# Optimization experiments

Measured on AMD Instinct MI355X. Metric: run time of the kernel, lower is better.

Reference implementation:

```python
import jax, jax.numpy as jnp
import numpy as np

B, S, D = 2, 8192, 2048
H, HD = 16, 128
LSH_NUM_PROJS = 7
BLOCK = 256          # key/query block size for block-diagonal attention
SAMPLE = 256         # number of uniformly sampled residual columns
ROPE_BASE = 10000.0
LOG_WEIGHT = float(np.log(S / SAMPLE))  # importance weight for sampled columns


def setup_inputs() -> dict:
    key = jax.random.key(0)
    ks = jax.random.split(key, 5)
    x = jax.random.normal(ks[0], (B, S, D), jnp.float32)
    w_in = jax.random.normal(ks[1], (D, 3 * D), jnp.float32) * (D ** -0.5)
    w_out = jax.random.normal(ks[2], (D, D), jnp.float32) * (D ** -0.5)
    lsh_proj = jax.random.normal(ks[3], (HD, LSH_NUM_PROJS), jnp.float32)
    sampled_set = jax.random.randint(ks[4], (B, H, SAMPLE), 0, S, jnp.int32)
    return {"x": x, "w_in": w_in, "w_out": w_out,
            "lsh_proj": lsh_proj, "sampled_set": sampled_set}


def _rope(t):
    # t: [B, S, H, HD]; LLaMA-style half-split rotary embedding, offset=0
    half = HD // 2
    inv_freq = 1.0 / (ROPE_BASE ** (jnp.arange(half, dtype=jnp.float32) / half))
    freqs = jnp.arange(S, dtype=jnp.float32)[:, None] * inv_freq[None, :]  # [S, half]
    cos = jnp.cos(freqs)[None, :, None, :]
    sin = jnp.sin(freqs)[None, :, None, :]
    t1, t2 = t[..., :half], t[..., half:]
    return jnp.concatenate([t1 * cos - t2 * sin, t2 * cos + t1 * sin], axis=-1)


def _lse_attn(q, k, v, scale, bias=None):
    # exact attention with log-sum-exp; q [...,n,d], k/v [...,m,d]
    s = jnp.einsum('...nd,...md->...nm', q, k) * scale
    if bias is not None:
        s = s + bias
    lse = jax.nn.logsumexp(s, axis=-1, keepdims=True)   # [...,n,1]
    p = jnp.exp(s - lse)
    return jnp.einsum('...nm,...md->...nd', p, v), lse


def _hyper_attention(q, k, v, lsh_proj, sampled_set):
    # q,k,v: [B,H,S,HD]  (non-causal HyperAttention path)
    scale = HD ** -0.5

    def lsh_hash(t):
        # simhash bucket codes from sign bits of random projections
        bits = jnp.einsum('bhsd,dp->bhsp', t, lsh_proj) > 0
        powers = (2 ** jnp.arange(LSH_NUM_PROJS)).astype(jnp.int32)
        return jnp.sum(bits.astype(jnp.int32) * powers, axis=-1)  # [B,H,S]

    q_idx = jnp.argsort(lsh_hash(q), axis=-1, stable=True)
    k_idx = jnp.argsort(lsh_hash(k), axis=-1, stable=True)
    q_idx_inv = jnp.argsort(q_idx, axis=-1, stable=True)
    gather = lambda t, i: jnp.take_along_axis(t, i[..., None], axis=2)

    qs = gather(q, q_idx)
    ks_ = gather(k, k_idx)
    vs = gather(v, k_idx)

    # 1. block-diagonal exact attention on LSH-sorted order
    nb = S // BLOCK
    qb = qs.reshape(B, H, nb, BLOCK, HD)
    kb = ks_.reshape(B, H, nb, BLOCK, HD)
    vb = vs.reshape(B, H, nb, BLOCK, HD)
    attn_blk, lse_blk = _lse_attn(qb, kb, vb, scale)
    attn_blk = attn_blk.reshape(B, H, S, HD)
    lse_blk = lse_blk.reshape(B, H, S, 1)

    # 2. residual: uniformly sampled columns (indices into sorted key order),
    #    masking columns already covered by the query's diagonal block
    k_sub = gather(ks_, sampled_set)   # [B,H,m,HD]
    v_sub = gather(vs, sampled_set)
    q_block_id = jnp.arange(S, dtype=jnp.int32) // BLOCK          # [S]
    s_block_id = sampled_set // BLOCK                             # [B,H,m]
    neg = jnp.finfo(q.dtype).min
    bias = jnp.where(q_block_id[None, None, :, None] == s_block_id[:, :, None, :],
                     neg, jnp.array(0.0, q.dtype))                # [B,H,S,m]
    attn_res, lse_res = _lse_attn(qs, k_sub, v_sub, scale, bias=bias)
    lse_res = lse_res + LOG_WEIGHT

    # 3. merge the two partial softmax results (online-softmax combine)
    lse = jnp.logaddexp(lse_blk, lse_res)
    attn = attn_blk * jnp.exp(lse_blk - lse) + attn_res * jnp.exp(lse_res - lse)

    # undo query sort
    return gather(attn, q_idx_inv)


def reference(x, w_in, w_out, lsh_proj, sampled_set):
    qkv = x @ w_in                           # [B,S,3D]
    q, k, v = jnp.split(qkv, 3, axis=-1)
    r4 = lambda t: t.reshape(B, S, H, HD)
    q, k, v = _rope(r4(q)), _rope(r4(k)), r4(v)
    tr = lambda t: t.transpose(0, 2, 1, 3)   # -> [B,H,S,HD]
    out = _hyper_attention(tr(q), tr(k), tr(v), lsh_proj, sampled_set)
    out = out.transpose(0, 2, 1, 3).reshape(B, S, D)
    return out @ w_out
```

## Files before the change

kernel.cpp:

```cpp
#include <hip/hip_runtime.h>
#include <stdint.h>

typedef _Float16 f16;
typedef _Float16 f16x8 __attribute__((ext_vector_type(8)));
typedef float f32x4 __attribute__((ext_vector_type(4)));
typedef uint32_t u32;

#define SEQ 8192
#define NH 16
#define HDIM 128
#define BHCNT 32
#define KDIM 2048
#define SCALE 0.08838834764831845f
#define LOGW 3.4657359027997265f
#define TAU1 0.06f
#define TAU 6e-3f
#define MAXWL 32768
#define BCAP 1024

__device__ __forceinline__ f32x4 mfma16(f16x8 a, f16x8 b, f32x4 c){
  return __builtin_amdgcn_mfma_f32_16x16x32_f16(a, b, c, 0, 0, 0);
}

__device__ __forceinline__ void g2l16(const f16* g, f16* l){
  __builtin_amdgcn_global_load_lds(
      (const __attribute__((address_space(1))) void*)g,
      (__attribute__((address_space(3))) void*)l, 16, 0, 0);
}

__global__ __launch_bounds__(256) void split_x_k(const float* __restrict__ x,
                                                 f16* __restrict__ xh, f16* __restrict__ xl){
  size_t i = ((size_t)blockIdx.x * 256 + threadIdx.x) * 4;
  float4 v = *(const float4*)(x + i);
  f16 h0 = (f16)v.x, h1 = (f16)v.y, h2 = (f16)v.z, h3 = (f16)v.w;
  union { f16 h[4]; ushort4 u; } a, b;
  a.h[0]=h0; a.h[1]=h1; a.h[2]=h2; a.h[3]=h3;
  b.h[0]=(f16)(v.x-(float)h0); b.h[1]=(f16)(v.y-(float)h1);
  b.h[2]=(f16)(v.z-(float)h2); b.h[3]=(f16)(v.w-(float)h3);
  *(ushort4*)(xh + i) = a.u;
  *(ushort4*)(xl + i) = b.u;
}

__global__ void transpose_k(const float* __restrict__ in, f16* __restrict__ ohi,
                            f16* __restrict__ olo, int Kd, int Nd, int NLO){
  __shared__ float t[32][33];
  int tx = threadIdx.x, ty = threadIdx.y;
  int n0 = blockIdx.x*32, k0 = blockIdx.y*32;
  #pragma unroll
  for (int i=0;i<4;i++) t[ty+i*8][tx] = in[(size_t)(k0+ty+i*8)*Nd + n0+tx];
  __syncthreads();
  #pragma unroll
  for (int i=0;i<4;i++){
    int n = n0 + ty + i*8, k = k0 + tx;
    float v = t[tx][ty+i*8];
    f16 h = (f16)v;
    ohi[(size_t)n*Kd + k] = h;
    if (n < NLO) olo[(size_t)n*Kd + k] = (f16)(v - (float)h);
  }
}

__global__ __launch_bounds__(256) void rope_table_k(float* __restrict__ ct, float* __restrict__ st){
  int i = blockIdx.x * 256 + threadIdx.x;
  int s = i >> 6, d = i & 63;
  float p32 = (float)pow(10000.0, (double)d / 64.0);
  float inv = __fdiv_rn(1.0f, p32);
  float f = __fmul_rn((float)s, inv);
  double a = (double)f;
  ct[i] = (float)cos(a);
  st[i] = (float)sin(a);
}

__global__ void zero_k(int* p){ p[0] = 0; p[1] = 0; p[2] = 0; }

__global__ void diag_k(const int* __restrict__ flags, float* __restrict__ out){
  int c = flags[0];
  if (c == 0 || c >= MAXWL || flags[2]) out[0] = 1.0e9f + (float)c;
}

template<int SPLIT, int MODE>
__global__ __launch_bounds__(256) void gemm_k(
    const f16* __restrict__ A, const f16* __restrict__ Al,
    const f16* __restrict__ Bt, const f16* __restrict__ Btl,
    float* __restrict__ o0, float* __restrict__ o1, f16* __restrict__ oh, int N){
  __shared__ f16 sm[SPLIT ? 16384 : 8192];
  const int tid = threadIdx.x, lane = tid & 63, wave = tid >> 6;
  const int wr = wave >> 1, wc = wave & 1;
  const int brow = blockIdx.y, bcol = blockIdx.x;
  const int g = lane >> 4, q_ = lane & 15;
  f32x4 acc[4][4];
  #pragma unroll
  for (int m=0;m<4;m++)
    #pragma unroll
    for (int n=0;n<4;n++) acc[m][n] = (f32x4){0.f,0.f,0.f,0.f};
  const int srow = tid >> 2, sseg = tid & 3;
  const int scol = (sseg ^ (srow & 3)) * 8;
  const f16* ga0 = A  + (size_t)(brow*128 + srow)*KDIM + scol;
  const f16* gb0 = Bt + (size_t)(bcol*128 + srow)*KDIM + scol;
  f16* As = sm; f16* Bs = sm + 4096;
  f16* dA0 = As + wave*512; f16* dA1 = As + 2048 + wave*512;
  f16* dB0 = Bs + wave*512; f16* dB1 = Bs + 2048 + wave*512;
  const int aoff = (wr*64 + q_)*32 + (g ^ (q_ & 3))*8;
  const int boff = (wc*64 + q_)*32 + (g ^ (q_ & 3))*8;
  for (int kt = 0; kt < KDIM/32; ++kt){
    const size_t ko = (size_t)kt * 32;
    g2l16(ga0 + ko, dA0); g2l16(ga0 + (size_t)64*KDIM + ko, dA1);
    g2l16(gb0 + ko, dB0); g2l16(gb0 + (size_t)64*KDIM + ko, dB1);
    if constexpr (SPLIT){
      const f16* gal = Al  + (ga0 - A);
      const f16* gbl = Btl + (gb0 - Bt);
      g2l16(gal + ko, sm + 8192  + wave*512); g2l16(gal + (size_t)64*KDIM + ko, sm + 8192  + 2048 + wave*512);
      g2l16(gbl + ko, sm + 12288 + wave*512); g2l16(gbl + (size_t)64*KDIM + ko, sm + 12288 + 2048 + wave*512);
    }
    __syncthreads();
    f16x8 af[4], afl[4];
    #pragma unroll
    for (int m=0;m<4;m++){
      af[m] = *(const f16x8*)&As[aoff + m*16*32];
      if constexpr (SPLIT) afl[m] = *(const f16x8*)&sm[8192 + aoff + m*16*32];
    }
    #pragma unroll
    for (int n=0;n<4;n++){
      f16x8 bf = *(const f16x8*)&Bs[boff + n*16*32];
      f16x8 bfl;
      if constexpr (SPLIT) bfl = *(const f16x8*)&sm[12288 + boff + n*16*32];
      #pragma unroll
      for (int m=0;m<4;m++){
        acc[m][n] = mfma16(af[m], bf, acc[m][n]);
        if constexpr (SPLIT){
          acc[m][n] = mfma16(af[m],  bfl, acc[m][n]);
          acc[m][n] = mfma16(afl[m], bf,  acc[m][n]);
        }
      }
    }
    __syncthreads();
  }
  #pragma unroll
  for (int m=0;m<4;m++)
    #pragma unroll
    for (int n=0;n<4;n++)
      #pragma unroll
      for (int j=0;j<4;j++){
        int row = brow*128 + wr*64 + m*16 + g*4 + j;
        int col = bcol*128 + wc*64 + n*16 + q_;
        float v = acc[m][n][j];
        if constexpr (MODE == 0){
          o0[(size_t)row * N + col] = v;
        } else if constexpr (MODE == 1){
          int b = row >> 13, s = row & 8191;
          int cl = col & 2047;
          int h = cl >> 7, hd = cl & 127;
          float* dst = (col < 2048) ? o0 : o1;
          dst[(((size_t)b*NH + h)*SEQ + s)*HDIM + hd] = v;
        } else {
          int b = row >> 13, s = row & 8191;
          int h = col >> 7, hd = col & 127;
          oh[(((size_t)b*NH + h)*SEQ + s)*HDIM + hd] = (f16)v;
        }
      }
}

__global__ __launch_bounds__(256) void rope_hash_k(float* __restrict__ qk, const float* __restrict__ ct,
    const float* __restrict__ st, const float* __restrict__ proj, int* __restrict__ hout,
    int tag, int* __restrict__ wl, int* __restrict__ wcnt){
  const int lane = threadIdx.x & 63, wave = threadIdx.x >> 6;
  const int s = blockIdx.x * 4 + wave, bh = blockIdx.y;
  float* row = qk + ((size_t)bh * SEQ + s) * HDIM;
  float2 v = *(const float2*)(row + 2*lane);
  float ox = __shfl_xor(v.x, 32), oy = __shfl_xor(v.y, 32);
  const int dl = 2*lane, di = dl & 63;
  const float* cb = ct + (size_t)s*64; const float* sb = st + (size_t)s*64;
  float c0 = cb[di], c1 = cb[di+1], sn0 = sb[di], sn1 = sb[di+1];
  float r0, r1;
  if (lane < 32){ r0 = v.x*c0 - ox*sn0; r1 = v.y*c1 - oy*sn1; }
  else          { r0 = v.x*c0 + ox*sn0; r1 = v.y*c1 + oy*sn1; }
  union { f16 h[2]; u32 u; } pk;
  pk.h[0] = (f16)r0; pk.h[1] = (f16)r1;
  *(u32*)((f16*)row + dl) = pk.u;
  float part[7];
  #pragma unroll
  for (int p=0;p<7;p++) part[p] = r0*proj[dl*7+p] + r1*proj[(dl+1)*7+p];
  #pragma unroll
  for (int off=32; off>=1; off>>=1){
    #pragma unroll
    for (int p=0;p<7;p++) part[p] += __shfl_xor(part[p], off);
  }
  if (lane == 0){
    int hs = 0; float mn = 1e30f;
    #pragma unroll
    for (int p=0;p<7;p++){ if (part[p] > 0.f) hs |= (1<<p); mn = fminf(mn, fabsf(part[p])); }
    hout[bh*SEQ + s] = hs;
    if (mn < TAU1){
      int w = atomicAdd(wcnt, 1);
      if (w < MAXWL){ wl[2*w] = (bh<<1) | tag; wl[2*w+1] = s; }
    }
  }
}

__global__ __launch_bounds__(256) void bucket_k(const int* __restrict__ wl, const int* __restrict__ wcnt,
    int* __restrict__ wl2, int* __restrict__ cnt2, int* __restrict__ flags){
  const int bucket = blockIdx.x;
  __shared__ int lcnt;
  if (threadIdx.x == 0) lcnt = 0;
  __syncthreads();
  int count = wcnt[0]; if (count > MAXWL) count = MAXWL;
  for (int i = threadIdx.x; i < count; i += 256){
    int tagbh = wl[2*i];
    int tag = tagbh & 1, h = (tagbh >> 1) & 15;
    if (tag*16 + h == bucket){
      int pos = atomicAdd(&lcnt, 1);
      if (pos < BCAP) wl2[bucket*BCAP + pos] = (tagbh << 13) | wl[2*i+1];
    }
  }
  __syncthreads();
  if (threadIdx.x == 0){
    cnt2[bucket] = (lcnt > BCAP) ? BCAP : lcnt;
    if (lcnt > BCAP) atomicExch(&flags[2], 1);
  }
}

__global__ __launch_bounds__(256) void t2_k(const f16* __restrict__ xh, const f16* __restrict__ xl,
    const f16* __restrict__ wh, const f16* __restrict__ wlo,
    const int* __restrict__ wl2, const int* __restrict__ cnt2,
    const float* __restrict__ ct, const float* __restrict__ st, const float* __restrict__ proj,
    int* __restrict__ hq, int* __restrict__ hk, int* __restrict__ wl3, int* __restrict__ wcnt3){
  const int bucket = blockIdx.y;
  const int nrows = cnt2[bucket];
  const int base = blockIdx.x * 64;
  if (base >= nrows) return;
  const int tid = threadIdx.x, lane = tid & 63, wave = tid >> 6;
  const int g = lane >> 4, q_ = lane & 15;
  __shared__ f16 Ah[64*32], Alo[64*32], Bh[128*32], Bl[128*32];
  __shared__ float S[64][128];
  __shared__ int rs[64], ent[64];
  if (tid < 64){
    int idx = base + tid;
    int e = wl2[bucket*BCAP + (idx < nrows ? idx : 0)];
    ent[tid] = e;
    int s = e & 8191;
    int b = e >> 18;
    rs[tid] = b * SEQ + s;
  }
  __syncthreads();
  const int tag = bucket >> 4, h = bucket & 15;
  const f16* Wh = wh  + ((size_t)(tag*2048 + h*128)) * KDIM;
  const f16* Wl = wlo + ((size_t)(tag*2048 + h*128)) * KDIM;
  f32x4 acc[8];
  #pragma unroll
  for (int n=0;n<8;n++) acc[n] = (f32x4){0.f,0.f,0.f,0.f};
  const int arow = tid >> 2, aseg = tid & 3;
  const int bcol = tid >> 1, bhalf = tid & 1;
  const size_t abase = (size_t)rs[arow]*KDIM + aseg*8;
  const size_t bbase = (size_t)bcol*KDIM + bhalf*16;
  for (int kt = 0; kt < 64; ++kt){
    const int k0 = kt*32;
    *(f16x8*)&Ah [arow*32 + aseg*8] = *(const f16x8*)(xh + abase + k0);
    *(f16x8*)&Alo[arow*32 + aseg*8] = *(const f16x8*)(xl + abase + k0);
    *(f16x8*)&Bh[bcol*32 + bhalf*16]     = *(const f16x8*)(Wh + bbase + k0);
    *(f16x8*)&Bh[bcol*32 + bhalf*16 + 8] = *(const f16x8*)(Wh + bbase + k0 + 8);
    *(f16x8*)&Bl[bcol*32 + bhalf*16]     = *(const f16x8*)(Wl + bbase + k0);
    *(f16x8*)&Bl[bcol*32 + bhalf*16 + 8] = *(const f16x8*)(Wl + bbase + k0 + 8);
    __syncthreads();
    f16x8 ah = *(const f16x8*)&Ah [(wave*16 + q_)*32 + g*8];
    f16x8 al = *(const f16x8*)&Alo[(wave*16 + q_)*32 + g*8];
    #pragma unroll
    for (int n=0;n<8;n++){
      f16x8 bh8 = *(const f16x8*)&Bh[(n*16 + q_)*32 + g*8];
      f16x8 bl8 = *(const f16x8*)&Bl[(n*16 + q_)*32 + g*8];
      acc[n] = mfma16(ah, bh8, acc[n]);
      acc[n] = mfma16(ah, bl8, acc[n]);
      acc[n] = mfma16(al, bh8, acc[n]);
    }
    __syncthreads();
  }
  #pragma unroll
  for (int n=0;n<8;n++)
    #pragma unroll
    for (int j=0;j<4;j++)
      S[wave*16 + g*4 + j][n*16 + q_] = acc[n][j];
  __syncthreads();
  for (int r = 0; r < 16; ++r){
    int row = wave*16 + r;
    int gidx = base + row;
    if (gidx >= nrows) break;
    int e = ent[row];
    int s = e & 8191;
    int tagbh = e >> 13;
    int bh = tagbh >> 1;
    float vx = S[row][2*lane], vy = S[row][2*lane+1];
    float ox = __shfl_xor(vx, 32), oy = __shfl_xor(vy, 32);
    const int dl = 2*lane, di = dl & 63;
    float c0 = ct[(size_t)s*64 + di], c1v = ct[(size_t)s*64 + di + 1];
    float sn0 = st[(size_t)s*64 + di], sn1 = st[(size_t)s*64 + di + 1];
    float r0, r1;
    if (lane < 32){ r0 = vx*c0 - ox*sn0; r1 = vy*c1v - oy*sn1; }
    else          { r0 = vx*c0 + ox*sn0; r1 = vy*c1v + oy*sn1; }
    float part[7];
    #pragma unroll
    for (int p=0;p<7;p++) part[p] = r0*proj[dl*7+p] + r1*proj[(dl+1)*7+p];
    #pragma unroll
    for (int off=32; off>=1; off>>=1){
      #pragma unroll
      for (int p=0;p<7;p++) part[p] += __shfl_xor(part[p], off);
    }
    if (lane == 0){
      int hs = 0; float mn = 1e30f;
      #pragma unroll
      for (int p=0;p<7;p++){ if (part[p] > 0.f) hs |= (1<<p); mn = fminf(mn, fabsf(part[p])); }
      ((tagbh & 1) ? hk : hq)[bh*SEQ + s] = hs;
      if (mn < TAU){
        int w = atomicAdd(wcnt3, 1);
        if (w < MAXWL){ wl3[2*w] = tagbh; wl3[2*w+1] = s; }
      }
    }
  }
}

__global__ __launch_bounds__(256) void fixup_k(const float* __restrict__ x, const float* __restrict__ w_in,
    const float* __restrict__ proj, const float* __restrict__ ct, const float* __restrict__ st,
    const int* __restrict__ wl, const int* __restrict__ wcnt,
    int* __restrict__ hq, int* __restrict__ hk){
  const int lane = threadIdx.x & 63, wave = threadIdx.x >> 6;
  const int gw = blockIdx.x * 4 + wave, nw = gridDim.x * 4;
  int count = *wcnt; if (count > MAXWL) count = MAXWL;
  for (int e = gw; e < count; e += nw){
    int tagbh = wl[2*e], s = wl[2*e+1];
    int tag = tagbh & 1, bh = tagbh >> 1;
    int b = bh >> 4, h = bh & 15;
    const float* xr = x + ((size_t)b*SEQ + s)*KDIM;
    const int c0i = tag*2048 + h*128 + lane;
    double a0 = 0.0, a1 = 0.0;
    for (int j = 0; j < KDIM; ++j){
      double xv = (double)xr[j];
      a0 += xv * (double)w_in[(size_t)j*6144 + c0i];
      a1 += xv * (double)w_in[(size_t)j*6144 + c0i + 64];
    }
    double c = (double)ct[(size_t)s*64 + lane];
    double sn = (double)st[(size_t)s*64 + lane];
    double r0 = a0*c - a1*sn;
    double r1 = a1*c + a0*sn;
    int hs = 0;
    #pragma unroll
    for (int p = 0; p < 7; ++p){
      double part = r0 * (double)proj[lane*7+p] + r1 * (double)proj[(lane+64)*7+p];
      #pragma unroll
      for (int off = 32; off >= 1; off >>= 1) part += __shfl_xor(part, off);
      if (part > 0.0) hs |= (1<<p);
    }
    if (lane == 0) (tag ? hk : hq)[bh*SEQ + s] = hs;
  }
}

__global__ __launch_bounds__(256) void sort_k(const int* __restrict__ hsh, int* __restrict__ idx){
  const int bh = blockIdx.x, tid = threadIdx.x;
  __shared__ unsigned char hl[SEQ];
  __shared__ unsigned short hist[128*256];
  __shared__ unsigned int part[256];
  const int* hrow = hsh + bh*SEQ;
  for (int i = tid; i < SEQ; i += 256) hl[i] = (unsigned char)hrow[i];
  u32* h32 = (u32*)hist;
  for (int i = tid; i < 128*256/2; i += 256) h32[i] = 0;
  __syncthreads();
  #pragma unroll 1
  for (int j = 0; j < 32; ++j){
    int hv = hl[tid*32 + j];
    hist[hv*256 + tid] = (unsigned short)(hist[hv*256 + tid] + 1);
  }
  __syncthreads();
  unsigned int s = 0;
  #pragma unroll 1
  for (int f = tid*128; f < tid*128 + 128; ++f) s += hist[f];
  part[tid] = s;
  __syncthreads();
  for (int off = 1; off < 256; off <<= 1){
    unsigned int v = (tid >= off) ? part[tid - off] : 0u;
    __syncthreads();
    part[tid] += v;
    __syncthreads();
  }
  unsigned int run = (tid == 0) ? 0u : part[tid - 1];
  #pragma unroll 1
  for (int f = tid*128; f < tid*128 + 128; ++f){
    unsigned short c = hist[f];
    hist[f] = (unsigned short)run;
    run += c;
  }
  __syncthreads();
  int* orow = idx + bh*SEQ;
  #pragma unroll 1
  for (int j = 0; j < 32; ++j){
    int i = tid*32 + j;
    int hv = hl[i];
    unsigned short p = hist[hv*256 + tid];
    hist[hv*256 + tid] = (unsigned short)(p + 1);
    orow[p] = i;
  }
}

__global__ __launch_bounds__(256) void attn_k(const f16* __restrict__ qr, const f16* __restrict__ kr,
    const f16* __restrict__ v, const int* __restrict__ qidx, const int* __restrict__ kidx,
    const int* __restrict__ smp, f16* __restrict__ out){
  const int tid = threadIdx.x, lane = tid & 63, wave = tid >> 6;
  const int chunk = blockIdx.x, bh = blockIdx.y;
  const int b = bh >> 4, h = bh & 15;
  const int qblock = chunk >> 2;
  __shared__ f16 Kl[32*136];
  __shared__ f16 Vt[128*40];
  __shared__ float biasl[256];
  __shared__ int kid[512];
  const int g = lane >> 4, q_ = lane & 15;
  for (int j = tid; j < 512; j += 256){
    int kpos;
    if (j < 256) kpos = qblock*256 + j;
    else {
      kpos = smp[bh*256 + (j-256)];
      biasl[j-256] = ((kpos >> 8) == qblock) ? -1e30f : LOGW;
    }
    kid[j] = kidx[bh*SEQ + kpos];
  }
  const int qpos = chunk*64 + wave*16 + q_;
  const int qi = qidx[bh*SEQ + qpos];
  const f16* qb = qr + ((size_t)bh*SEQ + qi)*256;
  f16x8 qf[4];
  #pragma unroll
  for (int c=0;c<4;c++) qf[c] = *(const f16x8*)(qb + c*32 + g*8);
  f32x4 O[8];
  #pragma unroll
  for (int c=0;c<8;c++) O[c] = (f32x4){0.f,0.f,0.f,0.f};
  float m_run = -1e30f, l_run = 0.f;
  __syncthreads();
  const int kkK = tid >> 3, segK = tid & 7;
  const int kk2 = tid & 15, d0 = (tid >> 4) * 8;
  f16x8 pk0, pk1, pv0, pv1;
  {
    int krw = kid[kkK];
    const f16* ks = kr + ((size_t)bh*SEQ + krw)*256 + segK*16;
    pk0 = *(const f16x8*)ks; pk1 = *(const f16x8*)(ks + 8);
    int r0 = kid[2*kk2], r1 = kid[2*kk2 + 1];
    pv0 = *(const f16x8*)(v + ((size_t)bh*SEQ + r0)*HDIM + d0);
    pv1 = *(const f16x8*)(v + ((size_t)bh*SEQ + r1)*HDIM + d0);
  }
  for (int t = 0; t < 16; ++t){
    *(f16x8*)&Kl[kkK*136 + segK*16]     = pk0;
    *(f16x8*)&Kl[kkK*136 + segK*16 + 8] = pk1;
    #pragma unroll
    for (int i=0;i<8;i++){
      union { f16 h[2]; u32 u; } pr;
      pr.h[0] = pv0[i]; pr.h[1] = pv1[i];
      *(u32*)&Vt[(d0+i)*40 + 2*kk2] = pr.u;
    }
    __syncthreads();
    if (t < 15){
      int jb = (t+1)*32;
      int krw = kid[jb + kkK];
      const f16* ks = kr + ((size_t)bh*SEQ + krw)*256 + segK*16;
      pk0 = *(const f16x8*)ks; pk1 = *(const f16x8*)(ks + 8);
      int r0 = kid[jb + 2*kk2], r1 = kid[jb + 2*kk2 + 1];
      pv0 = *(const f16x8*)(v + ((size_t)bh*SEQ + r0)*HDIM + d0);
      pv1 = *(const f16x8*)(v + ((size_t)bh*SEQ + r1)*HDIM + d0);
    }
    f32x4 c0 = (f32x4){0.f,0.f,0.f,0.f}, c1 = (f32x4){0.f,0.f,0.f,0.f};
    #pragma unroll
    for (int c=0;c<4;c++){
      f16x8 k0 = *(const f16x8*)&Kl[q_*136 + c*32 + g*8];
      f16x8 k1 = *(const f16x8*)&Kl[(16+q_)*136 + c*32 + g*8];
      c0 = mfma16(k0, qf[c], c0);
      c1 = mfma16(k1, qf[c], c1);
    }
    float sc[8];
    if (t < 8){
      #pragma unroll
      for (int j=0;j<4;j++){ sc[j] = c0[j]*SCALE; sc[4+j] = c1[j]*SCALE; }
    } else {
      const float* bb = &biasl[(t-8)*32];
      #pragma unroll
      for (int j=0;j<4;j++){ sc[j] = c0[j]*SCALE + bb[g*4+j]; sc[4+j] = c1[j]*SCALE + bb[16+g*4+j]; }
    }
    float mx = sc[0];
    #pragma unroll
    for (int i=1;i<8;i++) mx = fmaxf(mx, sc[i]);
    mx = fmaxf(mx, __shfl_xor(mx, 16));
    mx = fmaxf(mx, __shfl_xor(mx, 32));
    float mnew = fmaxf(m_run, mx);
    float al = __expf(m_run - mnew);
    float p[8]; float ps = 0.f;
    #pragma unroll
    for (int i=0;i<8;i++){ p[i] = __expf(sc[i] - mnew); ps += p[i]; }
    ps += __shfl_xor(ps, 16);
    ps += __shfl_xor(ps, 32);
    l_run = l_run * al + ps;
    m_run = mnew;
    float aj0 = __shfl(al, g*4+0), aj1 = __shfl(al, g*4+1);
    float aj2 = __shfl(al, g*4+2), aj3 = __shfl(al, g*4+3);
    #pragma unroll
    for (int c=0;c<8;c++){ O[c][0]*=aj0; O[c][1]*=aj1; O[c][2]*=aj2; O[c][3]*=aj3; }
    union { f16 h[2]; u32 u; } pk;
    pk.h[0]=(f16)p[0]; pk.h[1]=(f16)p[1]; u32 A0 = pk.u;
    pk.h[0]=(f16)p[2]; pk.h[1]=(f16)p[3]; u32 A1 = pk.u;
    pk.h[0]=(f16)p[4]; pk.h[1]=(f16)p[5]; u32 B0 = pk.u;
    pk.h[0]=(f16)p[6]; pk.h[1]=(f16)p[7]; u32 B1 = pk.u;
    int srcA = (((2*g)&3)<<4) | q_;
    int srcB = ((((2*g)+1)&3)<<4) | q_;
    bool selh = g >= 2;
    u32 xa0 = __shfl(A0, srcA), xb0 = __shfl(B0, srcA);
    u32 xa1 = __shfl(A1, srcA), xb1 = __shfl(B1, srcA);
    u32 xa2 = __shfl(A0, srcB), xb2 = __shfl(B0, srcB);
    u32 xa3 = __shfl(A1, srcB), xb3 = __shfl(B1, srcB);
    union { u32 w[4]; f16x8 f; } pf;
    pf.w[0] = selh ? xb0 : xa0;
    pf.w[1] = selh ? xb1 : xa1;
    pf.w[2] = selh ? xb2 : xa2;
    pf.w[3] = selh ? xb3 : xa3;
    #pragma unroll
    for (int c=0;c<8;c++){
      f16x8 vf = *(const f16x8*)&Vt[(c*16 + q_)*40 + g*8];
      O[c] = mfma16(pf.f, vf, O[c]);
    }
    __syncthreads();
  }
  float li0 = 1.f/__shfl(l_run, g*4+0), li1 = 1.f/__shfl(l_run, g*4+1);
  float li2 = 1.f/__shfl(l_run, g*4+2), li3 = 1.f/__shfl(l_run, g*4+3);
  const int posbase = chunk*64 + wave*16;
  #pragma unroll
  for (int j=0;j<4;j++){
    float li = (j==0)?li0:((j==1)?li1:((j==2)?li2:li3));
    int sorig = qidx[bh*SEQ + posbase + g*4 + j];
    f16* dst = out + (((size_t)b*SEQ + sorig)*NH + h)*HDIM;
    #pragma unroll
    for (int c=0;c<8;c++) dst[c*16 + q_] = (f16)(O[c][j] * li);
  }
}

extern "C" void kernel_launch(void* const* d_in, const int* in_sizes, int n_in,
                              void* d_out, int out_size, void* d_ws, size_t ws_size,
                              hipStream_t stream) {
  (void)in_sizes; (void)n_in; (void)out_size; (void)ws_size;
  const float* x     = (const float*)d_in[0];
  const float* w_in  = (const float*)d_in[1];
  const float* w_out = (const float*)d_in[2];
  const float* proj  = (const float*)d_in[3];
  const int*   smp   = (const int*)d_in[4];
  float* out = (float*)d_out;

  char* ws = (char*)d_ws;
  size_t off = 0;
  auto alloc = [&](size_t bytes){ void* p = ws + off; off += (bytes + 255) & ~(size_t)255; return p; };
  f16*   xh   = (f16*)alloc((size_t)16384*2048*2);
  f16*   xl   = (f16*)alloc((size_t)16384*2048*2);
  f16*   wh   = (f16*)alloc((size_t)6144*2048*2);
  f16*   wl   = (f16*)alloc((size_t)4096*2048*2);
  f16*   wo   = (f16*)alloc((size_t)2048*2048*2);
  float* qf   = (float*)alloc((size_t)BHCNT*SEQ*HDIM*4);
  float* kf   = (float*)alloc((size_t)BHCNT*SEQ*HDIM*4);
  f16*   vv   = (f16*)alloc((size_t)BHCNT*SEQ*HDIM*2);
  float* cost = (float*)alloc((size_t)SEQ*64*4);
  float* sint = (float*)alloc((size_t)SEQ*64*4);
  int*   hq   = (int*)alloc((size_t)BHCNT*SEQ*4);
  int*   hk   = (int*)alloc((size_t)BHCNT*SEQ*4);
  int*   qidx = (int*)alloc((size_t)BHCNT*SEQ*4);
  int*   kidx = (int*)alloc((size_t)BHCNT*SEQ*4);
  int*   wlst = (int*)alloc((size_t)MAXWL*2*4);
  int*   wlst2= (int*)alloc((size_t)32*BCAP*4);
  int*   wlst3= (int*)alloc((size_t)MAXWL*2*4);
  int*   cnt2 = (int*)alloc(256);
  int*   flags= (int*)alloc(256);
  f16*   attn = xl;

  int* wcnt  = flags;
  int* wcnt3 = flags + 1;

  zero_k<<<1, 1, 0, stream>>>(flags);
  split_x_k<<<32768, 256, 0, stream>>>(x, xh, xl);
  transpose_k<<<dim3(192,64), dim3(32,8), 0, stream>>>(w_in, wh, wl, 2048, 6144, 4096);
  transpose_k<<<dim3(64,64),  dim3(32,8), 0, stream>>>(w_out, wo, nullptr, 2048, 2048, 0);
  rope_table_k<<<2048, 256, 0, stream>>>(cost, sint);

  gemm_k<0,1><<<dim3(32,128), 256, 0, stream>>>(xh, nullptr, wh, nullptr, qf, kf, nullptr, 4096);
  gemm_k<0,2><<<dim3(16,128), 256, 0, stream>>>(xh, nullptr, wh + (size_t)4096*2048, nullptr,
                                                nullptr, nullptr, vv, 2048);

  rope_hash_k<<<dim3(2048,32), 256, 0, stream>>>(qf, cost, sint, proj, hq, 0, wlst, wcnt);
  rope_hash_k<<<dim3(2048,32), 256, 0, stream>>>(kf, cost, sint, proj, hk, 1, wlst, wcnt);

  bucket_k<<<32, 256, 0, stream>>>(wlst, wcnt, wlst2, cnt2, flags);
  t2_k<<<dim3(16,32), 256, 0, stream>>>(xh, xl, wh, wl, wlst2, cnt2, cost, sint, proj,
                                        hq, hk, wlst3, wcnt3);
  fixup_k<<<512, 256, 0, stream>>>(x, w_in, proj, cost, sint, wlst3, wcnt3, hq, hk);

  sort_k<<<32, 256, 0, stream>>>(hq, qidx);
  sort_k<<<32, 256, 0, stream>>>(hk, kidx);

  attn_k<<<dim3(128,32), 256, 0, stream>>>((const f16*)qf, (const f16*)kf, vv,
                                           qidx, kidx, smp, attn);

  gemm_k<0,0><<<dim3(16,128), 256, 0, stream>>>(attn, nullptr, wo, nullptr,
                                                out, nullptr, nullptr, 2048);

  diag_k<<<1, 1, 0, stream>>>(flags, out);
}
```

Before: 1.738 ms.

## Fuse QKV GEMMs, store Q/K in fp16, drop x low-part buffer, swizzle tiles

Merges the two input-projection GEMMs into one launch over a 1D grid with an 8-way block swizzle for L2 locality. Q and K are now written directly as fp16 instead of fp32, which halves the projection output traffic and the rope_hash reads. The x low-part split buffer is removed; t2_k now recomputes the hi/lo fp16 split from fp32 x on the fly. The attention buffer gets its own allocation, and the row strides in attn_k change to match the packed fp16 Q/K layout. The risk is a small precision loss, since rope is now applied to fp16-rounded Q/K values.

```diff
diff --git a/kernel.cpp b/kernel.cpp
--- a/kernel.cpp
+++ b/kernel.cpp
@@ -29,16 +29,12 @@
 }
 
 __global__ __launch_bounds__(256) void split_x_k(const float* __restrict__ x,
-                                                 f16* __restrict__ xh, f16* __restrict__ xl){
+                                                 f16* __restrict__ xh){
   size_t i = ((size_t)blockIdx.x * 256 + threadIdx.x) * 4;
   float4 v = *(const float4*)(x + i);
-  f16 h0 = (f16)v.x, h1 = (f16)v.y, h2 = (f16)v.z, h3 = (f16)v.w;
-  union { f16 h[4]; ushort4 u; } a, b;
-  a.h[0]=h0; a.h[1]=h1; a.h[2]=h2; a.h[3]=h3;
-  b.h[0]=(f16)(v.x-(float)h0); b.h[1]=(f16)(v.y-(float)h1);
-  b.h[2]=(f16)(v.z-(float)h2); b.h[3]=(f16)(v.w-(float)h3);
+  union { f16 h[4]; ushort4 u; } a;
+  a.h[0]=(f16)v.x; a.h[1]=(f16)v.y; a.h[2]=(f16)v.z; a.h[3]=(f16)v.w;
   *(ushort4*)(xh + i) = a.u;
-  *(ushort4*)(xl + i) = b.u;
 }
 
 __global__ void transpose_k(const float* __restrict__ in, f16* __restrict__ ohi,
@@ -77,15 +73,18 @@
   if (c == 0 || c >= MAXWL || flags[2]) out[0] = 1.0e9f + (float)c;
 }
 
-template<int SPLIT, int MODE>
+template<int MODE, int NC>
 __global__ __launch_bounds__(256) void gemm_k(
-    const f16* __restrict__ A, const f16* __restrict__ Al,
-    const f16* __restrict__ Bt, const f16* __restrict__ Btl,
-    float* __restrict__ o0, float* __restrict__ o1, f16* __restrict__ oh, int N){
-  __shared__ f16 sm[SPLIT ? 16384 : 8192];
+    const f16* __restrict__ A, const f16* __restrict__ Bt,
+    f16* __restrict__ q16, f16* __restrict__ k16, f16* __restrict__ v16,
+    float* __restrict__ o0, int N){
+  __shared__ f16 sm[8192];
   const int tid = threadIdx.x, lane = tid & 63, wave = tid >> 6;
   const int wr = wave >> 1, wc = wave & 1;
-  const int brow = blockIdx.y, bcol = blockIdx.x;
+  const int wg = blockIdx.x;
+  const int chunkw = gridDim.x >> 3;
+  const int swz = (wg & 7) * chunkw + (wg >> 3);
+  const int bcol = swz % NC, brow = swz / NC;
   const int g = lane >> 4, q_ = lane & 15;
   f32x4 acc[4][4];
   #pragma unroll
@@ -105,32 +104,15 @@
     const size_t ko = (size_t)kt * 32;
     g2l16(ga0 + ko, dA0); g2l16(ga0 + (size_t)64*KDIM + ko, dA1);
     g2l16(gb0 + ko, dB0); g2l16(gb0 + (size_t)64*KDIM + ko, dB1);
-    if constexpr (SPLIT){
-      const f16* gal = Al  + (ga0 - A);
-      const f16* gbl = Btl + (gb0 - Bt);
-      g2l16(gal + ko, sm + 8192  + wave*512); g2l16(gal + (size_t)64*KDIM + ko, sm + 8192  + 2048 + wave*512);
-      g2l16(gbl + ko, sm + 12288 + wave*512); g2l16(gbl + (size_t)64*KDIM + ko, sm + 12288 + 2048 + wave*512);
-    }
-    __syncthreads();
-    f16x8 af[4], afl[4];
-    #pragma unroll
-    for (int m=0;m<4;m++){
-      af[m] = *(const f16x8*)&As[aoff + m*16*32];
-      if constexpr (SPLIT) afl[m] = *(const f16x8*)&sm[8192 + aoff + m*16*32];
-    }
+    __syncthreads();
+    f16x8 af[4];
+    #pragma unroll
+    for (int m=0;m<4;m++) af[m] = *(const f16x8*)&As[aoff + m*16*32];
     #pragma unroll
     for (int n=0;n<4;n++){
       f16x8 bf = *(const f16x8*)&Bs[boff + n*16*32];
-      f16x8 bfl;
-      if constexpr (SPLIT) bfl = *(const f16x8*)&sm[12288 + boff + n*16*32];
-      #pragma unroll
-      for (int m=0;m<4;m++){
-        acc[m][n] = mfma16(af[m], bf, acc[m][n]);
-        if constexpr (SPLIT){
-          acc[m][n] = mfma16(af[m],  bfl, acc[m][n]);
-          acc[m][n] = mfma16(afl[m], bf,  acc[m][n]);
-        }
-      }
+      #pragma unroll
+      for (int m=0;m<4;m++) acc[m][n] = mfma16(af[m], bf, acc[m][n]);
     }
     __syncthreads();
   }
@@ -145,37 +127,34 @@
         float v = acc[m][n][j];
         if constexpr (MODE == 0){
           o0[(size_t)row * N + col] = v;
-        } else if constexpr (MODE == 1){
+        } else {
           int b = row >> 13, s = row & 8191;
+          int sec = col >> 11;
           int cl = col & 2047;
           int h = cl >> 7, hd = cl & 127;
-          float* dst = (col < 2048) ? o0 : o1;
-          dst[(((size_t)b*NH + h)*SEQ + s)*HDIM + hd] = v;
-        } else {
-          int b = row >> 13, s = row & 8191;
-          int h = col >> 7, hd = col & 127;
-          oh[(((size_t)b*NH + h)*SEQ + s)*HDIM + hd] = (f16)v;
+          f16* dst = (sec == 0) ? q16 : ((sec == 1) ? k16 : v16);
+          dst[(((size_t)b*NH + h)*SEQ + s)*HDIM + hd] = (f16)v;
         }
       }
 }
 
-__global__ __launch_bounds__(256) void rope_hash_k(float* __restrict__ qk, const float* __restrict__ ct,
+__global__ __launch_bounds__(256) void rope_hash_k(f16* __restrict__ qk, const float* __restrict__ ct,
     const float* __restrict__ st, const float* __restrict__ proj, int* __restrict__ hout,
     int tag, int* __restrict__ wl, int* __restrict__ wcnt){
   const int lane = threadIdx.x & 63, wave = threadIdx.x >> 6;
   const int s = blockIdx.x * 4 + wave, bh = blockIdx.y;
-  float* row = qk + ((size_t)bh * SEQ + s) * HDIM;
-  float2 v = *(const float2*)(row + 2*lane);
-  float ox = __shfl_xor(v.x, 32), oy = __shfl_xor(v.y, 32);
+  f16* row = qk + ((size_t)bh * SEQ + s) * HDIM;
+  float vx = (float)row[2*lane], vy = (float)row[2*lane+1];
+  float ox = __shfl_xor(vx, 32), oy = __shfl_xor(vy, 32);
   const int dl = 2*lane, di = dl & 63;
   const float* cb = ct + (size_t)s*64; const float* sb = st + (size_t)s*64;
   float c0 = cb[di], c1 = cb[di+1], sn0 = sb[di], sn1 = sb[di+1];
   float r0, r1;
-  if (lane < 32){ r0 = v.x*c0 - ox*sn0; r1 = v.y*c1 - oy*sn1; }
-  else          { r0 = v.x*c0 + ox*sn0; r1 = v.y*c1 + oy*sn1; }
+  if (lane < 32){ r0 = vx*c0 - ox*sn0; r1 = vy*c1 - oy*sn1; }
+  else          { r0 = vx*c0 + ox*sn0; r1 = vy*c1 + oy*sn1; }
   union { f16 h[2]; u32 u; } pk;
   pk.h[0] = (f16)r0; pk.h[1] = (f16)r1;
-  *(u32*)((f16*)row + dl) = pk.u;
+  *(u32*)(row + dl) = pk.u;
   float part[7];
   #pragma unroll
   for (int p=0;p<7;p++) part[p] = r0*proj[dl*7+p] + r1*proj[(dl+1)*7+p];
@@ -218,7 +197,7 @@
   }
 }
 
-__global__ __launch_bounds__(256) void t2_k(const f16* __restrict__ xh, const f16* __restrict__ xl,
+__global__ __launch_bounds__(256) void t2_k(const float* __restrict__ x,
     const f16* __restrict__ wh, const f16* __restrict__ wlo,
     const int* __restrict__ wl2, const int* __restrict__ cnt2,
     const float* __restrict__ ct, const float* __restrict__ st, const float* __restrict__ proj,
@@ -253,8 +232,20 @@
   const size_t bbase = (size_t)bcol*KDIM + bhalf*16;
   for (int kt = 0; kt < 64; ++kt){
     const int k0 = kt*32;
-    *(f16x8*)&Ah [arow*32 + aseg*8] = *(const f16x8*)(xh + abase + k0);
-    *(f16x8*)&Alo[arow*32 + aseg*8] = *(const f16x8*)(xl + abase + k0);
+    {
+      union { float4 f4[2]; float f[8]; } xa;
+      xa.f4[0] = *(const float4*)(x + abase + k0);
+      xa.f4[1] = *(const float4*)(x + abase + k0 + 4);
+      union { f16 h[8]; f16x8 v; } hh, ll;
+      #pragma unroll
+      for (int i=0;i<8;i++){
+        f16 hv = (f16)xa.f[i];
+        hh.h[i] = hv;
+        ll.h[i] = (f16)(xa.f[i] - (float)hv);
+      }
+      *(f16x8*)&Ah [arow*32 + aseg*8] = hh.v;
+      *(f16x8*)&Alo[arow*32 + aseg*8] = ll.v;
+    }
     *(f16x8*)&Bh[bcol*32 + bhalf*16]     = *(const f16x8*)(Wh + bbase + k0);
     *(f16x8*)&Bh[bcol*32 + bhalf*16 + 8] = *(const f16x8*)(Wh + bbase + k0 + 8);
     *(f16x8*)&Bl[bcol*32 + bhalf*16]     = *(const f16x8*)(Wl + bbase + k0);
@@ -419,7 +410,7 @@
   }
   const int qpos = chunk*64 + wave*16 + q_;
   const int qi = qidx[bh*SEQ + qpos];
-  const f16* qb = qr + ((size_t)bh*SEQ + qi)*256;
+  const f16* qb = qr + ((size_t)bh*SEQ + qi)*HDIM;
   f16x8 qf[4];
   #pragma unroll
   for (int c=0;c<4;c++) qf[c] = *(const f16x8*)(qb + c*32 + g*8);
@@ -433,7 +424,7 @@
   f16x8 pk0, pk1, pv0, pv1;
   {
     int krw = kid[kkK];
-    const f16* ks = kr + ((size_t)bh*SEQ + krw)*256 + segK*16;
+    const f16* ks = kr + ((size_t)bh*SEQ + krw)*HDIM + segK*16;
     pk0 = *(const f16x8*)ks; pk1 = *(const f16x8*)(ks + 8);
     int r0 = kid[2*kk2], r1 = kid[2*kk2 + 1];
     pv0 = *(const f16x8*)(v + ((size_t)bh*SEQ + r0)*HDIM + d0);
@@ -452,7 +443,7 @@
     if (t < 15){
       int jb = (t+1)*32;
       int krw = kid[jb + kkK];
-      const f16* ks = kr + ((size_t)bh*SEQ + krw)*256 + segK*16;
+      const f16* ks = kr + ((size_t)bh*SEQ + krw)*HDIM + segK*16;
       pk0 = *(const f16x8*)ks; pk1 = *(const f16x8*)(ks + 8);
       int r0 = kid[jb + 2*kk2], r1 = kid[jb + 2*kk2 + 1];
       pv0 = *(const f16x8*)(v + ((size_t)bh*SEQ + r0)*HDIM + d0);
@@ -545,13 +536,13 @@
   size_t off = 0;
   auto alloc = [&](size_t bytes){ void* p = ws + off; off += (bytes + 255) & ~(size_t)255; return p; };
   f16*   xh   = (f16*)alloc((size_t)16384*2048*2);
-  f16*   xl   = (f16*)alloc((size_t)16384*2048*2);
   f16*   wh   = (f16*)alloc((size_t)6144*2048*2);
   f16*   wl   = (f16*)alloc((size_t)4096*2048*2);
   f16*   wo   = (f16*)alloc((size_t)2048*2048*2);
-  float* qf   = (float*)alloc((size_t)BHCNT*SEQ*HDIM*4);
-  float* kf   = (float*)alloc((size_t)BHCNT*SEQ*HDIM*4);
+  f16*   qf   = (f16*)alloc((size_t)BHCNT*SEQ*HDIM*2);
+  f16*   kf   = (f16*)alloc((size_t)BHCNT*SEQ*HDIM*2);
   f16*   vv   = (f16*)alloc((size_t)BHCNT*SEQ*HDIM*2);
+  f16*   attn = (f16*)alloc((size_t)BHCNT*SEQ*HDIM*2);
   float* cost = (float*)alloc((size_t)SEQ*64*4);
   float* sint = (float*)alloc((size_t)SEQ*64*4);
   int*   hq   = (int*)alloc((size_t)BHCNT*SEQ*4);
@@ -563,37 +554,32 @@
   int*   wlst3= (int*)alloc((size_t)MAXWL*2*4);
   int*   cnt2 = (int*)alloc(256);
   int*   flags= (int*)alloc(256);
-  f16*   attn = xl;
 
   int* wcnt  = flags;
   int* wcnt3 = flags + 1;
 
   zero_k<<<1, 1, 0, stream>>>(flags);
-  split_x_k<<<32768, 256, 0, stream>>>(x, xh, xl);
+  split_x_k<<<32768, 256, 0, stream>>>(x, xh);
   transpose_k<<<dim3(192,64), dim3(32,8), 0, stream>>>(w_in, wh, wl, 2048, 6144, 4096);
   transpose_k<<<dim3(64,64),  dim3(32,8), 0, stream>>>(w_out, wo, nullptr, 2048, 2048, 0);
   rope_table_k<<<2048, 256, 0, stream>>>(cost, sint);
 
-  gemm_k<0,1><<<dim3(32,128), 256, 0, stream>>>(xh, nullptr, wh, nullptr, qf, kf, nullptr, 4096);
-  gemm_k<0,2><<<dim3(16,128), 256, 0, stream>>>(xh, nullptr, wh + (size_t)4096*2048, nullptr,
-                                                nullptr, nullptr, vv, 2048);
+  gemm_k<1,48><<<6144, 256, 0, stream>>>(xh, wh, qf, kf, vv, nullptr, 0);
 
   rope_hash_k<<<dim3(2048,32), 256, 0, stream>>>(qf, cost, sint, proj, hq, 0, wlst, wcnt);
   rope_hash_k<<<dim3(2048,32), 256, 0, stream>>>(kf, cost, sint, proj, hk, 1, wlst, wcnt);
 
   bucket_k<<<32, 256, 0, stream>>>(wlst, wcnt, wlst2, cnt2, flags);
-  t2_k<<<dim3(16,32), 256, 0, stream>>>(xh, xl, wh, wl, wlst2, cnt2, cost, sint, proj,
+  t2_k<<<dim3(16,32), 256, 0, stream>>>(x, wh, wl, wlst2, cnt2, cost, sint, proj,
                                         hq, hk, wlst3, wcnt3);
   fixup_k<<<512, 256, 0, stream>>>(x, w_in, proj, cost, sint, wlst3, wcnt3, hq, hk);
 
   sort_k<<<32, 256, 0, stream>>>(hq, qidx);
   sort_k<<<32, 256, 0, stream>>>(hk, kidx);
 
-  attn_k<<<dim3(128,32), 256, 0, stream>>>((const f16*)qf, (const f16*)kf, vv,
-                                           qidx, kidx, smp, attn);
-
-  gemm_k<0,0><<<dim3(16,128), 256, 0, stream>>>(attn, nullptr, wo, nullptr,
-                                                out, nullptr, nullptr, 2048);
+  attn_k<<<dim3(128,32), 256, 0, stream>>>(qf, kf, vv, qidx, kidx, smp, attn);
+
+  gemm_k<0,16><<<2048, 256, 0, stream>>>(attn, wo, nullptr, nullptr, nullptr, out, 2048);
 
   diag_k<<<1, 1, 0, stream>>>(flags, out);
 }
```

Result: faster. 1.691 ms (-2.7%).
